# Optimization experiments

Measured on AMD Instinct MI355X. Metric: run time of the kernel, lower is better.

## Reference

```python
import jax, jax.numpy as jnp
import numpy as np

G, N, DEG = 64, 2048, 8          # graphs, nodes/graph, avg degree
NTOT = G * N                      # 131072 nodes
E = NTOT * DEG                    # 1048576 edges
K = int(np.ceil(0.2 * N))         # 410 nodes kept per graph (SAGPooling ratio=0.2)
NK = G * K                        # 26240 pooled nodes
H, C = 3, 20                      # GAT heads, per-head channels
NEG_BIG = jnp.float32(-1e30)


def gcn(x, src, dst, W, b, n):
    """PyG GCNConv: x' = D^-1/2 (A+I) D^-1/2 x W + b (edge weight 1)."""
    h = x @ W
    deg = jax.ops.segment_sum(jnp.ones(src.shape[0], x.dtype), dst, num_segments=n) + 1.0
    dinv = jax.lax.rsqrt(deg)
    coef = dinv[src] * dinv[dst]                    # [E]
    agg = jax.ops.segment_sum(h[src] * coef[:, None], dst, num_segments=n)
    agg = agg + h * (dinv * dinv)[:, None]          # self loops
    return agg + b


def setup_inputs() -> dict:
    key = jax.random.key(0)
    ks = jax.random.split(key, 16)
    # edges constrained within each graph: per-graph local indices + offsets
    off = jnp.repeat(jnp.arange(G, dtype=jnp.int32) * N, N * DEG)   # [E]
    src = jax.random.randint(ks[0], (E,), 0, N, dtype=jnp.int32) + off
    dst = jax.random.randint(ks[1], (E,), 0, N, dtype=jnp.int32) + off
    batch = jnp.repeat(jnp.arange(G, dtype=jnp.int32), N)           # [NTOT]
    x = jax.random.normal(ks[2], (NTOT, 5), jnp.float32)
    s = 0.1
    return {
        "x": x, "src": src, "dst": dst, "batch": batch,
        "W1": jax.random.normal(ks[3], (5, 10)) * s,   "b1": jnp.zeros((10,)),
        "Ws": jax.random.normal(ks[4], (10, 1)) * s,   "bs": jnp.zeros((1,)),
        "Wg": jax.random.normal(ks[5], (10, H * C)) * s,
        "a_src": jax.random.normal(ks[6], (H, C)) * s,
        "a_dst": jax.random.normal(ks[7], (H, C)) * s,
        "bg": jnp.zeros((H * C,)),
        "Wf1": jax.random.normal(ks[8], (60, 30)) * s, "bf1": jnp.zeros((30,)),
        "Wf2": jax.random.normal(ks[9], (30, 3)) * s,  "bf2": jnp.zeros((3,)),
    }


def reference(x, src, dst, batch, W1, b1, Ws, bs, Wg, a_src, a_dst, bg, Wf1, bf1, Wf2, bf2):
    n = x.shape[0]
    # GCNConv(5,10)
    x1 = gcn(x, src, dst, W1, b1, n)                              # [NTOT,10]
    # SAGPooling: GCN scorer, top-k per graph, gate by tanh(score)
    score = gcn(x1, src, dst, Ws, bs, n)[:, 0]                    # [NTOT]
    _, topi = jax.lax.top_k(score.reshape(G, N), K)               # [G,K]
    perm = (topi + (jnp.arange(G) * N)[:, None]).reshape(-1)      # [NK] global ids
    xp = x1[perm] * jnp.tanh(score[perm])[:, None]                # [NK,10]
    # remap edges; drop (mask) edges touching removed nodes (filter_adj)
    new_idx = jnp.full((n,), -1, jnp.int32).at[perm].set(jnp.arange(NK, dtype=jnp.int32))
    s2, d2 = new_idx[src], new_idx[dst]
    emask = (s2 >= 0) & (d2 >= 0)
    s2 = jnp.where(emask, s2, 0)
    d2 = jnp.where(emask, d2, 0)
    # GATConv(10, 20, heads=3) with self loops
    h = (xp @ Wg).reshape(NK, H, C)
    al_s = jnp.sum(h * a_src, -1)                                 # [NK,H]
    al_d = jnp.sum(h * a_dst, -1)
    loop = jnp.arange(NK, dtype=jnp.int32)
    sa = jnp.concatenate([s2, loop])
    da = jnp.concatenate([d2, loop])
    ma = jnp.concatenate([emask, jnp.ones((NK,), bool)])
    logits = jax.nn.leaky_relu(al_s[sa] + al_d[da], 0.2)          # [E+NK,H]
    logits = jnp.where(ma[:, None], logits, NEG_BIG)
    mx = jax.ops.segment_max(logits, da, num_segments=NK)         # finite: self loops
    w = jnp.exp(logits - mx[da]) * ma[:, None]
    denom = jax.ops.segment_sum(w, da, num_segments=NK)
    alpha = w / denom[da]                                         # edge softmax
    out = jax.ops.segment_sum(h[sa] * alpha[..., None], da, num_segments=NK)  # [NK,H,C]
    xg = out.reshape(NK, H * C) + bg                              # concat heads -> 60
    # scatter_add readout over graphs
    g = jax.ops.segment_sum(xg, batch[perm], num_segments=G)      # [G,60]
    # MLP + LogSoftmax
    z = jax.nn.relu(g @ Wf1 + bf1) @ Wf2 + bf2                    # [G,3]
    return jax.nn.log_softmax(z, axis=1)
```

## Files before the change

kernel.cpp:

```cpp
#include <hip/hip_runtime.h>
#include <math.h>

#define G    64
#define NPG  2048
#define NTOT (G * NPG)
#define EPG  (NPG * 8)
#define KSEL 410
#define NH   3
#define NC   20
#define HC   60
#define FCAP 24
#define KPAD 512
#define RP   12

#define OFF_H1P   0
#define OFF_XP    0
#define OFF_FADJ  16400
#define OFF_FCNT  36080
#define OFF_HF    37728
#define OFF_CSR   98304
#define OFF_HIST  131072
#define OFF_RS    139264
#define OFF_ALS   139264
#define OFF_ALD   144184
#define OFF_SK    147456
#define OFF_WRED  149104
#define OFF_GOUT  151024
#define OFF_HID   151264
#define OFF_NEWL  155648
#define OFF_PERML 159744
#define OFF_WSUM  160568
#define OFF_FLAGS 160632
#define ARENA_SZ  160648

__device__ inline float leaky(float x) { return x >= 0.f ? x : 0.2f * x; }

__device__ inline int wave_incl_scan(int v) {
    int lane = threadIdx.x & 63;
#pragma unroll
    for (int d = 1; d < 64; d <<= 1) {
        int t = __shfl_up(v, d, 64);
        if (lane >= d) v += t;
    }
    return v;
}

__global__ __launch_bounds__(1024, 4) void k_all(
    const float* __restrict__ x, const int* __restrict__ src, const int* __restrict__ dst,
    const float* __restrict__ W1, const float* __restrict__ b1,
    const float* __restrict__ Ws, const float* __restrict__ bs,
    const float* __restrict__ Wg, const float* __restrict__ a_srcw,
    const float* __restrict__ a_dstw, const float* __restrict__ bg,
    const float* __restrict__ Wf1, const float* __restrict__ bf1,
    const float* __restrict__ Wf2, const float* __restrict__ bf2,
    float* __restrict__ out)
{
    __shared__ __align__(16) char arena[ARENA_SZ];
    float*          h1p   = (float*)(arena + OFF_H1P);
    float*          xpL   = (float*)(arena + OFF_XP);
    unsigned short* fadjL = (unsigned short*)(arena + OFF_FADJ);
    int*            fcntL = (int*)(arena + OFF_FCNT);
    float*          hfL   = (float*)(arena + OFF_HF);
    unsigned short* csrL  = (unsigned short*)(arena + OFF_CSR);
    int*            hist  = (int*)(arena + OFF_HIST);
    float*          prB   = (float*)(arena + OFF_HIST);
    int*            rsL   = (int*)(arena + OFF_RS);
    float*          alsL  = (float*)(arena + OFF_ALS);
    float*          aldL  = (float*)(arena + OFF_ALD);
    unsigned*       skL   = (unsigned*)(arena + OFF_SK);
    float*          wred  = (float*)(arena + OFF_WRED);
    float*          goutL = (float*)(arena + OFF_GOUT);
    float*          hidL  = (float*)(arena + OFF_HID);
    unsigned short* newLs = (unsigned short*)(arena + OFF_NEWL);
    unsigned short* permL = (unsigned short*)(arena + OFF_PERML);
    int*            wsumL = (int*)(arena + OFF_WSUM);
    int*            flags = (int*)(arena + OFF_FLAGS);
#define bselS  flags[0]
#define bneedS flags[1]

    int g = blockIdx.x, tid = threadIdx.x, wid = tid >> 6;
    int nbase = g * NPG, ebase = g * EPG;

    for (int i = tid; i < NPG; i += 1024) hist[i] = 0;
    for (int i = tid; i < NPG; i += 1024) {
        float xi[5];
#pragma unroll
        for (int k = 0; k < 5; k++) xi[k] = x[(size_t)(nbase + i) * 5 + k];
        float v[10];
#pragma unroll
        for (int j = 0; j < 10; j++) {
            float s = 0.f;
#pragma unroll
            for (int k = 0; k < 5; k++) s += xi[k] * W1[k * 10 + j];
            v[j] = s;
        }
        float4* row = (float4*)(h1p + i * RP);
        row[0] = make_float4(v[0], v[1], v[2], v[3]);
        row[1] = make_float4(v[4], v[5], v[6], v[7]);
        row[2] = make_float4(v[8], v[9], 0.f, 0.f);
    }
    __syncthreads();
    for (int e = tid; e < EPG; e += 1024)
        atomicAdd(&hist[dst[ebase + e] - nbase], 1);
    __syncthreads();
    {
        int b2 = tid * 2;
        int v0 = hist[b2], v1 = hist[b2 + 1];
        int s = v0 + v1;
        int incl = wave_incl_scan(s);
        if ((tid & 63) == 63) wsumL[wid] = incl;
        __syncthreads();
        int pre = 0;
#pragma unroll
        for (int w = 0; w < 16; w++) { int t = wsumL[w]; if (w < wid) pre += t; }
        int base = pre + incl - s;
        rsL[b2] = base;
        rsL[b2 + 1] = base + v0;
        h1p[b2 * RP + 10] = rsqrtf((float)v0 + 1.0f);
        h1p[(b2 + 1) * RP + 10] = rsqrtf((float)v1 + 1.0f);
        hist[b2] = 0; hist[b2 + 1] = 0;
    }
    __syncthreads();
    for (int e = tid; e < EPG; e += 1024) {
        int ee = ebase + e;
        int sl = src[ee] - nbase;
        int dl = dst[ee] - nbase;
        int pos = rsL[dl] + atomicAdd(&hist[dl], 1);
        csrL[pos] = (unsigned short)sl;
    }
    __syncthreads();

    {
        int i0 = tid, i1 = tid + 1024;
        int e0 = rsL[i0], e0e = rsL[i0 + 1];
        int e1 = rsL[i1], e1e = (i1 == NPG - 1) ? EPG : rsL[i1 + 1];
        float acc0[10], acc1[10];
#pragma unroll
        for (int j = 0; j < 10; j++) { acc0[j] = 0.f; acc1[j] = 0.f; }
        while (e0 < e0e || e1 < e1e) {
            if (e0 < e0e) {
                int s = csrL[e0++];
                const float4* rw = (const float4*)(h1p + s * RP);
                float4 r0 = rw[0], r1 = rw[1], r2 = rw[2];
                float dv = r2.z;
                acc0[0] += r0.x * dv; acc0[1] += r0.y * dv; acc0[2] += r0.z * dv; acc0[3] += r0.w * dv;
                acc0[4] += r1.x * dv; acc0[5] += r1.y * dv; acc0[6] += r1.z * dv; acc0[7] += r1.w * dv;
                acc0[8] += r2.x * dv; acc0[9] += r2.y * dv;
            }
            if (e1 < e1e) {
                int s = csrL[e1++];
                const float4* rw = (const float4*)(h1p + s * RP);
                float4 r0 = rw[0], r1 = rw[1], r2 = rw[2];
                float dv = r2.z;
                acc1[0] += r0.x * dv; acc1[1] += r0.y * dv; acc1[2] += r0.z * dv; acc1[3] += r0.w * dv;
                acc1[4] += r1.x * dv; acc1[5] += r1.y * dv; acc1[6] += r1.z * dv; acc1[7] += r1.w * dv;
                acc1[8] += r2.x * dv; acc1[9] += r2.y * dv;
            }
        }
        const float4* q0 = (const float4*)(h1p + i0 * RP);
        const float4* q1 = (const float4*)(h1p + i1 * RP);
        float4 s00 = q0[0], s01 = q0[1], s02 = q0[2];
        float4 s10 = q1[0], s11 = q1[1], s12 = q1[2];
        float di0 = s02.z, d20 = di0 * di0;
        float di1 = s12.z, d21 = di1 * di1;
        float b1r[10];
#pragma unroll
        for (int j = 0; j < 10; j++) b1r[j] = b1[j];
        float v0[10], v1[10];
        v0[0] = acc0[0] * di0 + s00.x * d20 + b1r[0];
        v0[1] = acc0[1] * di0 + s00.y * d20 + b1r[1];
        v0[2] = acc0[2] * di0 + s00.z * d20 + b1r[2];
        v0[3] = acc0[3] * di0 + s00.w * d20 + b1r[3];
        v0[4] = acc0[4] * di0 + s01.x * d20 + b1r[4];
        v0[5] = acc0[5] * di0 + s01.y * d20 + b1r[5];
        v0[6] = acc0[6] * di0 + s01.z * d20 + b1r[6];
        v0[7] = acc0[7] * di0 + s01.w * d20 + b1r[7];
        v0[8] = acc0[8] * di0 + s02.x * d20 + b1r[8];
        v0[9] = acc0[9] * di0 + s02.y * d20 + b1r[9];
        v1[0] = acc1[0] * di1 + s10.x * d21 + b1r[0];
        v1[1] = acc1[1] * di1 + s10.y * d21 + b1r[1];
        v1[2] = acc1[2] * di1 + s10.z * d21 + b1r[2];
        v1[3] = acc1[3] * di1 + s10.w * d21 + b1r[3];
        v1[4] = acc1[4] * di1 + s11.x * d21 + b1r[4];
        v1[5] = acc1[5] * di1 + s11.y * d21 + b1r[5];
        v1[6] = acc1[6] * di1 + s11.z * d21 + b1r[6];
        v1[7] = acc1[7] * di1 + s11.w * d21 + b1r[7];
        v1[8] = acc1[8] * di1 + s12.x * d21 + b1r[8];
        v1[9] = acc1[9] * di1 + s12.y * d21 + b1r[9];
        float hs0 = 0.f, hs1 = 0.f;
#pragma unroll
        for (int j = 0; j < 10; j++) { float w = Ws[j]; hs0 += v0[j] * w; hs1 += v1[j] * w; }
        __syncthreads();
        float4* w0 = (float4*)(h1p + i0 * RP);
        w0[0] = make_float4(v0[0], v0[1], v0[2], v0[3]);
        w0[1] = make_float4(v0[4], v0[5], v0[6], v0[7]);
        w0[2] = make_float4(v0[8], v0[9], di0, hs0);
        float4* w1 = (float4*)(h1p + i1 * RP);
        w1[0] = make_float4(v1[0], v1[1], v1[2], v1[3]);
        w1[1] = make_float4(v1[4], v1[5], v1[6], v1[7]);
        w1[2] = make_float4(v1[8], v1[9], di1, hs1);
        prB[i0] = hs0 * di0;
        prB[i1] = hs1 * di1;
    }
    __syncthreads();

    {
        float bsv = bs[0];
        int i0 = tid, i1 = tid + 1024;
        float2 own0 = *(const float2*)(h1p + i0 * RP + 10);
        float2 own1 = *(const float2*)(h1p + i1 * RP + 10);
        int e0 = rsL[i0], e0e = rsL[i0 + 1];
        int e1 = rsL[i1], e1e = (i1 == NPG - 1) ? EPG : rsL[i1 + 1];
        float a0 = 0.f, a1 = 0.f;
        while (e0 < e0e || e1 < e1e) {
            if (e0 < e0e) a0 += prB[csrL[e0++]];
            if (e1 < e1e) a1 += prB[csrL[e1++]];
        }
        float sc0 = own0.x * a0 + own0.y * own0.x * own0.x + bsv;
        float sc1 = own1.x * a1 + own1.y * own1.x * own1.x + bsv;
        unsigned u0 = __float_as_uint(sc0);
        unsigned u1 = __float_as_uint(sc1);
        skL[i0] = (u0 & 0x80000000u) ? ~u0 : (u0 | 0x80000000u);
        skL[i1] = (u1 & 0x80000000u) ? ~u1 : (u1 | 0x80000000u);
        newLs[i0] = 0xFFFFu; newLs[i1] = 0xFFFFu;
    }
    int need = KSEL;
    unsigned prefix = 0;
    __syncthreads();
    for (int i = tid; i < NPG; i += 1024) hist[i] = 0;
    __syncthreads();

    for (int lv = 0; lv < 3; lv++) {
        for (int i = tid; i < NPG; i += 1024) {
            unsigned k = skL[i];
            bool match; unsigned bb;
            if (lv == 0)      { match = true;                  bb = k >> 21; }
            else if (lv == 1) { match = ((k >> 21) == prefix); bb = (k >> 10) & 0x7FFu; }
            else              { match = ((k >> 10) == prefix); bb = k & 0x3FFu; }
            if (match) atomicAdd(&hist[bb], 1);
        }
        __syncthreads();
        int b2 = tid * 2;
        int v0 = hist[b2], v1 = hist[b2 + 1];
        hist[b2] = 0; hist[b2 + 1] = 0;
        int s = v0 + v1;
        int incl = wave_incl_scan(s);
        if ((tid & 63) == 63) wsumL[wid] = incl;
        __syncthreads();
        int pre = 0, tot = 0;
#pragma unroll
        for (int w = 0; w < 16; w++) { int t = wsumL[w]; if (w < wid) pre += t; tot += t; }
        int base = pre + incl - s;
        { int Sb = tot - base;        int Sb1 = Sb - v0; if (Sb >= need && Sb1 < need) { bselS = b2;     bneedS = need - Sb1; } }
        { int Sb = tot - (base + v0); int Sb1 = Sb - v1; if (Sb >= need && Sb1 < need) { bselS = b2 + 1; bneedS = need - Sb1; } }
        __syncthreads();
        if (lv == 0)      prefix = (unsigned)bselS;
        else if (lv == 1) prefix = (prefix << 11) | (unsigned)bselS;
        else              prefix = (prefix << 10) | (unsigned)bselS;
        need = bneedS;
    }
    unsigned T = prefix;
    int greaterCnt = KSEL - need;

    {
        int b2 = tid * 2;
        unsigned k0 = skL[b2], k1 = skL[b2 + 1];
        int gt0 = k0 > T ? 1 : 0, gt1 = k1 > T ? 1 : 0;
        int eq0 = k0 == T ? 1 : 0, eq1 = k1 == T ? 1 : 0;
        int pack = ((gt0 + gt1) << 16) | (eq0 + eq1);
        int incl = wave_incl_scan(pack);
        if ((tid & 63) == 63) wsumL[wid] = incl;
        __syncthreads();
        int pre = 0;
#pragma unroll
        for (int w = 0; w < 16; w++) { int t = wsumL[w]; if (w < wid) pre += t; }
        int base = pre + incl - pack;
        int gb = base >> 16, eb = base & 0xFFFF;
        if (gt0) { permL[gb] = (unsigned short)b2; newLs[b2] = (unsigned short)gb; }
        if (gt1) { int r = gb + gt0; permL[r] = (unsigned short)(b2 + 1); newLs[b2 + 1] = (unsigned short)r; }
        if (eq0 && eb < need) { int p = greaterCnt + eb; permL[p] = (unsigned short)b2; newLs[b2] = (unsigned short)p; }
        if (eq1) { int r = eb + eq0; if (r < need) { int p = greaterCnt + r; permL[p] = (unsigned short)(b2 + 1); newLs[b2 + 1] = (unsigned short)p; } }
    }
    __syncthreads();

    {
        float4 rq0, rq1, rq2; float tt = 0.f;
        bool havep = (tid < KSEL);
        if (havep) {
            int iL = permL[tid];
            unsigned k = skL[iL];
            unsigned u = (k & 0x80000000u) ? (k & 0x7FFFFFFFu) : ~k;
            tt = tanhf(__uint_as_float(u));
            const float4* xr = (const float4*)(h1p + iL * RP);
            rq0 = xr[0]; rq1 = xr[1]; rq2 = xr[2];
        }
        __syncthreads();
        if (havep) {
            float* xp = xpL + tid * 10;
            xp[0] = rq0.x * tt; xp[1] = rq0.y * tt; xp[2] = rq0.z * tt; xp[3] = rq0.w * tt;
            xp[4] = rq1.x * tt; xp[5] = rq1.y * tt; xp[6] = rq1.z * tt; xp[7] = rq1.w * tt;
            xp[8] = rq2.x * tt; xp[9] = rq2.y * tt;
        }
    }
    __syncthreads();

    for (int p = tid; p < KSEL; p += 1024) {
        int iL = permL[p];
        int p0 = rsL[iL], p1 = (iL == NPG - 1) ? EPG : rsL[iL + 1];
        int c = 0;
        int e = p0;
        while (e < p1) {
            int n = p1 - e; n = n > 8 ? 8 : n;
            int b8[8];
#pragma unroll
            for (int j = 0; j < 8; j++) b8[j] = csrL[e + (j < n ? j : 0)];
            unsigned short n8[8];
#pragma unroll
            for (int j = 0; j < 8; j++) n8[j] = newLs[b8[j]];
#pragma unroll
            for (int j = 0; j < 8; j++)
                if (j < n && n8[j] != 0xFFFFu && c < FCAP) fadjL[p * FCAP + c++] = n8[j];
            e += n;
        }
        fcntL[p] = c;
    }
    __syncthreads();

    for (int t = tid; t < KSEL * NH; t += 1024) {
        int p = t / NH, hh = t - p * NH;
        float xi[10];
#pragma unroll
        for (int k = 0; k < 10; k++) xi[k] = xpL[p * 10 + k];
        float v[NC];
        float as_ = 0.f, ad_ = 0.f;
#pragma unroll
        for (int c = 0; c < NC; c++) {
            int j = hh * NC + c;
            float vv = 0.f;
#pragma unroll
            for (int k = 0; k < 10; k++) vv += xi[k] * Wg[k * HC + j];
            v[c] = vv;
            as_ += vv * a_srcw[j];
            ad_ += vv * a_dstw[j];
        }
        float4* hr = (float4*)(hfL + p * HC + hh * NC);
#pragma unroll
        for (int q = 0; q < 5; q++)
            hr[q] = make_float4(v[4 * q], v[4 * q + 1], v[4 * q + 2], v[4 * q + 3]);
        alsL[p * NH + hh] = as_;
        aldL[p * NH + hh] = ad_;
    }
    __syncthreads();

    {
        float res[NC];
#pragma unroll
        for (int rnd = 0; rnd < 2; rnd++) {
            int task = rnd == 0 ? tid : 1024 + tid;
            bool on = rnd == 0 || tid < KPAD;
            int hh = task >> 9, p = task & (KPAD - 1);
            if (on) {
                if (p < KSEL) {
                    float aldp = aldL[p * NH + hh];
                    float lself = leaky(alsL[p * NH + hh] + aldp);
                    int c = fcntL[p];
                    const float4* hp = (const float4*)(hfL + p * HC + hh * NC);
                    float4 r0 = hp[0], r1 = hp[1], r2 = hp[2], r3 = hp[3], r4 = hp[4];
                    float wsum = 1.f;
                    for (int e = 0; e < c; e++) {
                        int idx = fadjL[p * FCAP + e];
                        float w = __expf(leaky(alsL[idx * NH + hh] + aldp) - lself);
                        wsum += w;
                        const float4* hq = (const float4*)(hfL + idx * HC + hh * NC);
                        float4 t0 = hq[0], t1 = hq[1], t2 = hq[2], t3 = hq[3], t4 = hq[4];
                        r0.x += w * t0.x; r0.y += w * t0.y; r0.z += w * t0.z; r0.w += w * t0.w;
                        r1.x += w * t1.x; r1.y += w * t1.y; r1.z += w * t1.z; r1.w += w * t1.w;
                        r2.x += w * t2.x; r2.y += w * t2.y; r2.z += w * t2.z; r2.w += w * t2.w;
                        r3.x += w * t3.x; r3.y += w * t3.y; r3.z += w * t3.z; r3.w += w * t3.w;
                        r4.x += w * t4.x; r4.y += w * t4.y; r4.z += w * t4.z; r4.w += w * t4.w;
                    }
                    float inv = 1.f / wsum;
                    res[0] = r0.x * inv;  res[1] = r0.y * inv;  res[2] = r0.z * inv;  res[3] = r0.w * inv;
                    res[4] = r1.x * inv;  res[5] = r1.y * inv;  res[6] = r1.z * inv;  res[7] = r1.w * inv;
                    res[8] = r2.x * inv;  res[9] = r2.y * inv;  res[10] = r2.z * inv; res[11] = r2.w * inv;
                    res[12] = r3.x * inv; res[13] = r3.y * inv; res[14] = r3.z * inv; res[15] = r3.w * inv;
                    res[16] = r4.x * inv; res[17] = r4.y * inv; res[18] = r4.z * inv; res[19] = r4.w * inv;
                } else {
#pragma unroll
                    for (int cc = 0; cc < NC; cc++) res[cc] = 0.f;
                }
#pragma unroll
                for (int cc = 0; cc < NC; cc++) {
                    float v = res[cc];
#pragma unroll
                    for (int d = 1; d < 64; d <<= 1) v += __shfl_xor(v, d, 64);
                    res[cc] = v;
                }
                if ((tid & 63) == 0) {
                    int slot = rnd == 0 ? hh * 8 + (wid & 7) : 16 + wid;
#pragma unroll
                    for (int cc = 0; cc < NC; cc++) wred[slot * NC + cc] = res[cc];
                }
            }
        }
    }
    __syncthreads();
    if (tid < HC) {
        int hh = tid / NC, c = tid - hh * NC;
        float a = 0.f;
#pragma unroll
        for (int w = 0; w < 8; w++) a += wred[(hh * 8 + w) * NC + c];
        goutL[tid] = a + (float)KSEL * bg[tid];
    }
    __syncthreads();

    if (tid < 30) {
        float s = bf1[tid];
#pragma unroll
        for (int k = 0; k < HC; k++) s += goutL[k] * Wf1[k * 30 + tid];
        hidL[tid] = s > 0.f ? s : 0.f;
    }
    __syncthreads();
    if (tid == 0) {
        float z[3];
#pragma unroll
        for (int j = 0; j < 3; j++) {
            float s = bf2[j];
            for (int k = 0; k < 30; k++) s += hidL[k] * Wf2[k * 3 + j];
            z[j] = s;
        }
        float m = fmaxf(z[0], fmaxf(z[1], z[2]));
        float lse = logf(expf(z[0] - m) + expf(z[1] - m) + expf(z[2] - m)) + m;
#pragma unroll
        for (int j = 0; j < 3; j++) out[g * 3 + j] = z[j] - lse;
    }
}

extern "C" void kernel_launch(void* const* d_in, const int* in_sizes, int n_in,
                              void* d_out, int out_size, void* d_ws, size_t ws_size,
                              hipStream_t stream) {
    const float* x     = (const float*)d_in[0];
    const int*   src   = (const int*)d_in[1];
    const int*   dst   = (const int*)d_in[2];
    const float* W1    = (const float*)d_in[4];
    const float* b1    = (const float*)d_in[5];
    const float* Ws    = (const float*)d_in[6];
    const float* bs    = (const float*)d_in[7];
    const float* Wg    = (const float*)d_in[8];
    const float* a_src = (const float*)d_in[9];
    const float* a_dst = (const float*)d_in[10];
    const float* bg    = (const float*)d_in[11];
    const float* Wf1   = (const float*)d_in[12];
    const float* bf1   = (const float*)d_in[13];
    const float* Wf2   = (const float*)d_in[14];
    const float* bf2   = (const float*)d_in[15];
    float* out = (float*)d_out;
    (void)d_ws; (void)ws_size;

    k_all<<<G, 1024, 0, stream>>>(x, src, dst, W1, b1, Ws, bs, Wg, a_src, a_dst,
                                  bg, Wf1, bf1, Wf2, bf2, out);
}
```

Measured before the change: 141.7 us.

## Split fused per-graph kernel into three kernels with global workspace handoff

Splits the single monolithic per-graph kernel into three launches (GCN+score, top-k selection, GAT+readout), passing intermediate node features, keys, perm and remap through global workspace. It also rebuilds the filtered pooled adjacency by scanning the original edges with atomic appends instead of walking the CSR per kept node. The likely aim is to cut per-kernel shared memory and registers, and to make the adjacency build parallel over edges. In exchange it adds two extra launches and global-memory round trips, still with only 64 blocks per kernel. The atomic append also makes neighbor order nondeterministic.

```diff
diff --git a/kernel.cpp b/kernel.cpp
--- a/kernel.cpp
+++ b/kernel.cpp
@@ -3,7 +3,6 @@
 
 #define G    64
 #define NPG  2048
-#define NTOT (G * NPG)
 #define EPG  (NPG * 8)
 #define KSEL 410
 #define NH   3
@@ -13,25 +12,38 @@
 #define KPAD 512
 #define RP   12
 
-#define OFF_H1P   0
-#define OFF_XP    0
-#define OFF_FADJ  16400
-#define OFF_FCNT  36080
-#define OFF_HF    37728
-#define OFF_CSR   98304
-#define OFF_HIST  131072
-#define OFF_RS    139264
-#define OFF_ALS   139264
-#define OFF_ALD   144184
-#define OFF_SK    147456
-#define OFF_WRED  149104
-#define OFF_GOUT  151024
-#define OFF_HID   151264
-#define OFF_NEWL  155648
-#define OFF_PERML 159744
-#define OFF_WSUM  160568
-#define OFF_FLAGS 160632
-#define ARENA_SZ  160648
+#define WS_X1G  0
+#define WS_KEYS 6291456
+#define WS_PERM 6815744
+#define WS_NEWL 6881280
+
+#define A_H1P  0
+#define A_CSR  98304
+#define A_HIST 131072
+#define A_RS   139264
+#define A_WSUM 147456
+#define A_SZ   147520
+
+#define S_SK   0
+#define S_HIST 8192
+#define S_NEWL 16384
+#define S_PERM 20480
+#define S_WSUM 21504
+#define S_FLAG 21568
+#define S_SZ   21584
+
+#define E_XP    0
+#define E_FADJ  16400
+#define E_FCNT  36080
+#define E_HF    37728
+#define E_NEWL  37728
+#define E_PERM  41824
+#define E_ALS   136128
+#define E_ALD   141048
+#define E_WRED  145968
+#define E_GOUT  147888
+#define E_HID   148128
+#define E_SZ    148248
 
 __device__ inline float leaky(float x) { return x >= 0.f ? x : 0.2f * x; }
 
@@ -45,38 +57,19 @@
     return v;
 }
 
-__global__ __launch_bounds__(1024, 4) void k_all(
+__global__ __launch_bounds__(1024) void k_ab(
     const float* __restrict__ x, const int* __restrict__ src, const int* __restrict__ dst,
     const float* __restrict__ W1, const float* __restrict__ b1,
     const float* __restrict__ Ws, const float* __restrict__ bs,
-    const float* __restrict__ Wg, const float* __restrict__ a_srcw,
-    const float* __restrict__ a_dstw, const float* __restrict__ bg,
-    const float* __restrict__ Wf1, const float* __restrict__ bf1,
-    const float* __restrict__ Wf2, const float* __restrict__ bf2,
-    float* __restrict__ out)
+    float* __restrict__ x1g, unsigned* __restrict__ keysG)
 {
-    __shared__ __align__(16) char arena[ARENA_SZ];
-    float*          h1p   = (float*)(arena + OFF_H1P);
-    float*          xpL   = (float*)(arena + OFF_XP);
-    unsigned short* fadjL = (unsigned short*)(arena + OFF_FADJ);
-    int*            fcntL = (int*)(arena + OFF_FCNT);
-    float*          hfL   = (float*)(arena + OFF_HF);
-    unsigned short* csrL  = (unsigned short*)(arena + OFF_CSR);
-    int*            hist  = (int*)(arena + OFF_HIST);
-    float*          prB   = (float*)(arena + OFF_HIST);
-    int*            rsL   = (int*)(arena + OFF_RS);
-    float*          alsL  = (float*)(arena + OFF_ALS);
-    float*          aldL  = (float*)(arena + OFF_ALD);
-    unsigned*       skL   = (unsigned*)(arena + OFF_SK);
-    float*          wred  = (float*)(arena + OFF_WRED);
-    float*          goutL = (float*)(arena + OFF_GOUT);
-    float*          hidL  = (float*)(arena + OFF_HID);
-    unsigned short* newLs = (unsigned short*)(arena + OFF_NEWL);
-    unsigned short* permL = (unsigned short*)(arena + OFF_PERML);
-    int*            wsumL = (int*)(arena + OFF_WSUM);
-    int*            flags = (int*)(arena + OFF_FLAGS);
-#define bselS  flags[0]
-#define bneedS flags[1]
+    __shared__ __align__(16) char arena[A_SZ];
+    float*          h1p   = (float*)(arena + A_H1P);
+    unsigned short* csrL  = (unsigned short*)(arena + A_CSR);
+    int*            hist  = (int*)(arena + A_HIST);
+    float*          prB   = (float*)(arena + A_HIST);
+    int*            rsL   = (int*)(arena + A_RS);
+    int*            wsumL = (int*)(arena + A_WSUM);
 
     int g = blockIdx.x, tid = threadIdx.x, wid = tid >> 6;
     int nbase = g * NPG, ebase = g * EPG;
@@ -201,6 +194,10 @@
         w1[2] = make_float4(v1[8], v1[9], di1, hs1);
         prB[i0] = hs0 * di0;
         prB[i1] = hs1 * di1;
+        float4* g0 = (float4*)(x1g + (size_t)(nbase + i0) * RP);
+        g0[0] = w0[0]; g0[1] = w0[1]; g0[2] = make_float4(v0[8], v0[9], di0, hs0);
+        float4* g1 = (float4*)(x1g + (size_t)(nbase + i1) * RP);
+        g1[0] = w1[0]; g1[1] = w1[1]; g1[2] = make_float4(v1[8], v1[9], di1, hs1);
     }
     __syncthreads();
 
@@ -220,16 +217,36 @@
         float sc1 = own1.x * a1 + own1.y * own1.x * own1.x + bsv;
         unsigned u0 = __float_as_uint(sc0);
         unsigned u1 = __float_as_uint(sc1);
-        skL[i0] = (u0 & 0x80000000u) ? ~u0 : (u0 | 0x80000000u);
-        skL[i1] = (u1 & 0x80000000u) ? ~u1 : (u1 | 0x80000000u);
-        newLs[i0] = 0xFFFFu; newLs[i1] = 0xFFFFu;
+        keysG[nbase + i0] = (u0 & 0x80000000u) ? ~u0 : (u0 | 0x80000000u);
+        keysG[nbase + i1] = (u1 & 0x80000000u) ? ~u1 : (u1 | 0x80000000u);
+    }
+}
+
+__global__ __launch_bounds__(1024) void k_sel(
+    const unsigned* __restrict__ keysG, unsigned short* __restrict__ permG,
+    unsigned short* __restrict__ newlG)
+{
+    __shared__ __align__(16) char arena[S_SZ];
+    unsigned*       skL   = (unsigned*)(arena + S_SK);
+    int*            hist  = (int*)(arena + S_HIST);
+    unsigned short* newLs = (unsigned short*)(arena + S_NEWL);
+    unsigned short* permL = (unsigned short*)(arena + S_PERM);
+    int*            wsumL = (int*)(arena + S_WSUM);
+    int*            flags = (int*)(arena + S_FLAG);
+#define bselS  flags[0]
+#define bneedS flags[1]
+
+    int g = blockIdx.x, tid = threadIdx.x, wid = tid >> 6;
+    int nbase = g * NPG;
+
+    for (int i = tid; i < NPG; i += 1024) {
+        skL[i] = keysG[nbase + i];
+        newLs[i] = 0xFFFFu;
+        hist[i] = 0;
     }
     int need = KSEL;
     unsigned prefix = 0;
     __syncthreads();
-    for (int i = tid; i < NPG; i += 1024) hist[i] = 0;
-    __syncthreads();
-
     for (int lv = 0; lv < 3; lv++) {
         for (int i = tid; i < NPG; i += 1024) {
             unsigned k = skL[i];
@@ -261,7 +278,6 @@
     }
     unsigned T = prefix;
     int greaterCnt = KSEL - need;
-
     {
         int b2 = tid * 2;
         unsigned k0 = skL[b2], k1 = skL[b2 + 1];
@@ -282,47 +298,60 @@
         if (eq1) { int r = eb + eq0; if (r < need) { int p = greaterCnt + r; permL[p] = (unsigned short)(b2 + 1); newLs[b2 + 1] = (unsigned short)p; } }
     }
     __syncthreads();
-
-    {
-        float4 rq0, rq1, rq2; float tt = 0.f;
-        bool havep = (tid < KSEL);
-        if (havep) {
-            int iL = permL[tid];
-            unsigned k = skL[iL];
-            unsigned u = (k & 0x80000000u) ? (k & 0x7FFFFFFFu) : ~k;
-            tt = tanhf(__uint_as_float(u));
-            const float4* xr = (const float4*)(h1p + iL * RP);
-            rq0 = xr[0]; rq1 = xr[1]; rq2 = xr[2];
-        }
-        __syncthreads();
-        if (havep) {
-            float* xp = xpL + tid * 10;
-            xp[0] = rq0.x * tt; xp[1] = rq0.y * tt; xp[2] = rq0.z * tt; xp[3] = rq0.w * tt;
-            xp[4] = rq1.x * tt; xp[5] = rq1.y * tt; xp[6] = rq1.z * tt; xp[7] = rq1.w * tt;
-            xp[8] = rq2.x * tt; xp[9] = rq2.y * tt;
-        }
-    }
-    __syncthreads();
-
-    for (int p = tid; p < KSEL; p += 1024) {
-        int iL = permL[p];
-        int p0 = rsL[iL], p1 = (iL == NPG - 1) ? EPG : rsL[iL + 1];
-        int c = 0;
-        int e = p0;
-        while (e < p1) {
-            int n = p1 - e; n = n > 8 ? 8 : n;
-            int b8[8];
-#pragma unroll
-            for (int j = 0; j < 8; j++) b8[j] = csrL[e + (j < n ? j : 0)];
-            unsigned short n8[8];
-#pragma unroll
-            for (int j = 0; j < 8; j++) n8[j] = newLs[b8[j]];
-#pragma unroll
-            for (int j = 0; j < 8; j++)
-                if (j < n && n8[j] != 0xFFFFu && c < FCAP) fadjL[p * FCAP + c++] = n8[j];
-            e += n;
-        }
-        fcntL[p] = c;
+    for (int i = tid; i < NPG; i += 1024) newlG[nbase + i] = newLs[i];
+    if (tid < KSEL) permG[(size_t)g * 512 + tid] = permL[tid];
+}
+
+__global__ __launch_bounds__(1024) void k_efgh(
+    const int* __restrict__ src, const int* __restrict__ dst,
+    const float* __restrict__ x1g, const unsigned* __restrict__ keysG,
+    const unsigned short* __restrict__ permG, const unsigned short* __restrict__ newlG,
+    const float* __restrict__ Wg, const float* __restrict__ a_srcw,
+    const float* __restrict__ a_dstw, const float* __restrict__ bg,
+    const float* __restrict__ Wf1, const float* __restrict__ bf1,
+    const float* __restrict__ Wf2, const float* __restrict__ bf2,
+    float* __restrict__ out)
+{
+    __shared__ __align__(16) char arena[E_SZ];
+    float*          xpL   = (float*)(arena + E_XP);
+    unsigned short* fadjL = (unsigned short*)(arena + E_FADJ);
+    int*            fcntL = (int*)(arena + E_FCNT);
+    float*          hfL   = (float*)(arena + E_HF);
+    unsigned short* newLs = (unsigned short*)(arena + E_NEWL);
+    unsigned short* permL = (unsigned short*)(arena + E_PERM);
+    float*          alsL  = (float*)(arena + E_ALS);
+    float*          aldL  = (float*)(arena + E_ALD);
+    float*          wred  = (float*)(arena + E_WRED);
+    float*          goutL = (float*)(arena + E_GOUT);
+    float*          hidL  = (float*)(arena + E_HID);
+
+    int g = blockIdx.x, tid = threadIdx.x, wid = tid >> 6;
+    int nbase = g * NPG, ebase = g * EPG;
+
+    for (int i = tid; i < NPG; i += 1024) newLs[i] = newlG[nbase + i];
+    if (tid < KSEL) { permL[tid] = permG[(size_t)g * 512 + tid]; fcntL[tid] = 0; }
+    __syncthreads();
+
+    if (tid < KSEL) {
+        int iL = permL[tid];
+        unsigned k = keysG[nbase + iL];
+        unsigned u = (k & 0x80000000u) ? (k & 0x7FFFFFFFu) : ~k;
+        float tt = tanhf(__uint_as_float(u));
+        const float4* xr = (const float4*)(x1g + (size_t)(nbase + iL) * RP);
+        float4 q0 = xr[0], q1 = xr[1], q2 = xr[2];
+        float* xp = xpL + tid * 10;
+        xp[0] = q0.x * tt; xp[1] = q0.y * tt; xp[2] = q0.z * tt; xp[3] = q0.w * tt;
+        xp[4] = q1.x * tt; xp[5] = q1.y * tt; xp[6] = q1.z * tt; xp[7] = q1.w * tt;
+        xp[8] = q2.x * tt; xp[9] = q2.y * tt;
+    }
+    for (int e = tid; e < EPG; e += 1024) {
+        int ee = ebase + e;
+        unsigned short s2 = newLs[src[ee] - nbase];
+        unsigned short d2 = newLs[dst[ee] - nbase];
+        if (s2 != 0xFFFFu && d2 != 0xFFFFu) {
+            int c = atomicAdd(&fcntL[d2], 1);
+            if (c < FCAP) fadjL[d2 * FCAP + c] = s2;
+        }
     }
     __syncthreads();
 
@@ -363,7 +392,7 @@
                 if (p < KSEL) {
                     float aldp = aldL[p * NH + hh];
                     float lself = leaky(alsL[p * NH + hh] + aldp);
-                    int c = fcntL[p];
+                    int c = fcntL[p]; if (c > FCAP) c = FCAP;
                     const float4* hp = (const float4*)(hfL + p * HC + hh * NC);
                     float4 r0 = hp[0], r1 = hp[1], r2 = hp[2], r3 = hp[3], r4 = hp[4];
                     float wsum = 1.f;
@@ -455,8 +484,14 @@
     const float* Wf2   = (const float*)d_in[14];
     const float* bf2   = (const float*)d_in[15];
     float* out = (float*)d_out;
-    (void)d_ws; (void)ws_size;
-
-    k_all<<<G, 1024, 0, stream>>>(x, src, dst, W1, b1, Ws, bs, Wg, a_src, a_dst,
-                                  bg, Wf1, bf1, Wf2, bf2, out);
+
+    float*          x1g   = (float*)((char*)d_ws + WS_X1G);
+    unsigned*       keysG = (unsigned*)((char*)d_ws + WS_KEYS);
+    unsigned short* permG = (unsigned short*)((char*)d_ws + WS_PERM);
+    unsigned short* newlG = (unsigned short*)((char*)d_ws + WS_NEWL);
+
+    k_ab<<<G, 1024, 0, stream>>>(x, src, dst, W1, b1, Ws, bs, x1g, keysG);
+    k_sel<<<G, 1024, 0, stream>>>(keysG, permG, newlG);
+    k_efgh<<<G, 1024, 0, stream>>>(src, dst, x1g, keysG, permG, newlG,
+                                   Wg, a_src, a_dst, bg, Wf1, bf1, Wf2, bf2, out);
 }
```

After: 155.6 us. +9.8%, slower.
